# Performance work log

Measured on AMD Instinct MI355X. Metric: run time of the kernel, lower is better.

Reference implementation:

```python
import jax, jax.numpy as jnp
import numpy as np

B, T, C = 16, 2048, 384
E = 8          # num_experts
TOP_K = 2
CAP_F = 1.0
D_FF = 4 * C   # 1536


def setup_inputs() -> dict:
    key = jax.random.key(0)
    ks = jax.random.split(key, 10)
    s = 0.02
    return {
        "x": jax.random.normal(ks[0], (B, T, C), dtype=jnp.float32),
        "noise": jax.random.normal(ks[1], (B, T, E), dtype=jnp.float32),
        "w_route": jax.random.normal(ks[2], (C, E), dtype=jnp.float32) * s,
        "b_route": jnp.zeros((E,), dtype=jnp.float32),
        "w_noise": jax.random.normal(ks[3], (C, E), dtype=jnp.float32) * s,
        "b_noise": jnp.zeros((E,), dtype=jnp.float32),
        "w1": jax.random.normal(ks[4], (E, C, D_FF), dtype=jnp.float32) * s,
        "b1": jnp.zeros((E, D_FF), dtype=jnp.float32),
        "w2": jax.random.normal(ks[5], (E, D_FF, C), dtype=jnp.float32) * s,
        "b2": jnp.zeros((E, C), dtype=jnp.float32),
    }


def _moe_forward(x, noise, w_route, b_route, w_noise, b_noise, w1, b1, w2, b2):
    Bx, Tx, Cx = x.shape
    N = Bx * Tx
    cap = int(N * TOP_K / E * CAP_F)  # static expert capacity

    # --- NoisyTopkRouter ---
    logits = jnp.einsum('btc,ce->bte', x, w_route) + b_route
    noise_logits = jnp.einsum('btc,ce->bte', x, w_noise) + b_noise
    noisy = logits + noise * jax.nn.softplus(noise_logits)
    topv, topi = jax.lax.top_k(noisy, TOP_K)                    # [B,T,K]
    keep_mask = jnp.any(jax.nn.one_hot(topi, E, dtype=jnp.bool_), axis=-2)  # [B,T,E]
    sparse_logits = jnp.where(keep_mask, noisy, -jnp.inf)
    gating = jax.nn.softmax(sparse_logits, axis=-1)             # [B,T,E]

    # --- dispatch by top-1 expert with capacity drop (eval: dropout off) ---
    flat_x = x.reshape(N, Cx)
    flat_g = gating.reshape(N, E)
    top1 = jnp.argmax(flat_g, axis=-1)                          # [N]
    token_ids = jnp.arange(N, dtype=jnp.int32)
    out = jnp.zeros_like(flat_x)

    for i in range(E):
        mask = top1 == i                                        # [N]
        pos = jnp.cumsum(mask) - 1                              # rank within expert
        keep = mask & (pos < cap)
        slot = jnp.where(keep, pos, cap)                        # overflow -> dummy slot
        buf = jnp.zeros((cap + 1,), dtype=jnp.int32).at[slot].set(token_ids)
        idx = buf[:cap]                                         # token id per capacity slot
        valid = (jnp.arange(cap) < jnp.sum(keep))[:, None]      # [cap,1]
        xi = flat_x[idx]                                        # [cap,C] gather
        h = jnp.square(jax.nn.relu(xi @ w1[i] + b1[i]))         # ReLU^2
        yi = h @ w2[i] + b2[i]                                  # [cap,C]
        weighted = yi * flat_g[idx, i][:, None] * valid
        out = out.at[idx].add(weighted)                         # scatter-add

    return out.reshape(Bx, Tx, Cx)


def reference(x, noise, w_route, b_route, w_noise, b_noise, w1, b1, w2, b2):
    return _moe_forward(x, noise, w_route, b_route, w_noise, b_noise, w1, b1, w2, b2)
```

## Files before the change

kernel.cpp:

```cpp
#include <hip/hip_runtime.h>
#include <stdint.h>

#define E_NUM 8
#define CAP 8192
#define NTOK 32768
#define CDIM 384
#define DFF 1536
#define CNT_PAD 64

typedef unsigned short u16;
typedef __attribute__((ext_vector_type(8))) short short8;
typedef __attribute__((ext_vector_type(4))) float f32x4;

__device__ inline u16 f2bf(float f) {
    uint32_t u = __builtin_bit_cast(uint32_t, f);
    u += 0x7fffu + ((u >> 16) & 1u);
    return (u16)(u >> 16);
}

__device__ inline void gload_lds16(const void* g, void* l) {
    __builtin_amdgcn_global_load_lds(
        (const __attribute__((address_space(1))) void*)(uintptr_t)g,
        (__attribute__((address_space(3))) void*)(uint32_t)(uintptr_t)l,
        16, 0, 0);
}

__device__ inline void expert_span(const int* __restrict__ cnt, int e,
                                   int& base, int& n_e) {
    base = 0; n_e = 0;
#pragma unroll
    for (int i = 0; i < E_NUM; ++i) {
        int n = min(cnt[i * CNT_PAD], CAP);
        if (i < e) base += (n + 127) & ~127;
        else if (i == e) n_e = n;
    }
}

#define RT_TOK 64
#define RT_KC 64
#define RT_XS 68

__global__ __launch_bounds__(256, 4) void routing_kernel(
    const float* __restrict__ x, const float* __restrict__ noise,
    const float* __restrict__ w_route, const float* __restrict__ b_route,
    const float* __restrict__ w_noise, const float* __restrict__ b_noise,
    int* __restrict__ cnt, int* __restrict__ list, float* __restrict__ gate,
    u16* __restrict__ xbf)
{
    __shared__ float xs[RT_TOK * RT_XS];
    int tid = threadIdx.x;
    int lane = tid & 63;
    int seg = __builtin_amdgcn_readfirstlane(tid >> 6);
    int tok = tid & 63;
    int t0 = blockIdx.x * RT_TOK;

    int srow = tid >> 4;
    int scol = (tid & 15) * 4;

    float ar[E_NUM], an[E_NUM];
#pragma unroll
    for (int e = 0; e < E_NUM; ++e) { ar[e] = 0.f; an[e] = 0.f; }

    for (int c = 0; c < CDIM / RT_KC; ++c) {
        __syncthreads();
#pragma unroll
        for (int p = 0; p < 4; ++p) {
            int row = p * 16 + srow;
            float4 v = *(const float4*)(x + (size_t)(t0 + row) * CDIM + c * RT_KC + scol);
            *(float4*)&xs[row * RT_XS + scol] = v;
            uint2 b;
            b.x = (uint32_t)f2bf(v.x) | ((uint32_t)f2bf(v.y) << 16);
            b.y = (uint32_t)f2bf(v.z) | ((uint32_t)f2bf(v.w) << 16);
            *(uint2*)(xbf + (size_t)(t0 + row) * CDIM + c * RT_KC + scol) = b;
        }
        __syncthreads();
#pragma unroll
        for (int q = 0; q < 4; ++q) {
            float4 xq = *(const float4*)&xs[tok * RT_XS + seg * 16 + q * 4];
            int kb = c * RT_KC + seg * 16 + q * 4;
#pragma unroll
            for (int jj = 0; jj < 4; ++jj) {
                const float* wrk = w_route + (size_t)(kb + jj) * E_NUM;
                const float* wnk = w_noise + (size_t)(kb + jj) * E_NUM;
                float4 wa = *(const float4*)wrk, wb = *(const float4*)(wrk + 4);
                float4 na = *(const float4*)wnk, nb = *(const float4*)(wnk + 4);
                float xk = (jj == 0) ? xq.x : (jj == 1) ? xq.y : (jj == 2) ? xq.z : xq.w;
                ar[0] += xk * wa.x; ar[1] += xk * wa.y; ar[2] += xk * wa.z; ar[3] += xk * wa.w;
                ar[4] += xk * wb.x; ar[5] += xk * wb.y; ar[6] += xk * wb.z; ar[7] += xk * wb.w;
                an[0] += xk * na.x; an[1] += xk * na.y; an[2] += xk * na.z; an[3] += xk * na.w;
                an[4] += xk * nb.x; an[5] += xk * nb.y; an[6] += xk * nb.z; an[7] += xk * nb.w;
            }
        }
    }
    __syncthreads();
    float* part = xs;
    float* pp = part + (size_t)(seg * 64 + tok) * 16;
    *(f32x4*)&pp[0]  = (f32x4){ar[0], ar[1], ar[2], ar[3]};
    *(f32x4*)&pp[4]  = (f32x4){ar[4], ar[5], ar[6], ar[7]};
    *(f32x4*)&pp[8]  = (f32x4){an[0], an[1], an[2], an[3]};
    *(f32x4*)&pp[12] = (f32x4){an[4], an[5], an[6], an[7]};
    __syncthreads();
    if (seg == 0) {
        int t = t0 + lane;
        float sr[E_NUM], sn[E_NUM];
#pragma unroll
        for (int e = 0; e < E_NUM; ++e) { sr[e] = b_route[e]; sn[e] = b_noise[e]; }
#pragma unroll
        for (int s = 0; s < 4; ++s) {
            const float* q = part + (size_t)(s * 64 + lane) * 16;
#pragma unroll
            for (int e = 0; e < E_NUM; ++e) { sr[e] += q[e]; sn[e] += q[8 + e]; }
        }
        float nz[E_NUM];
        const float* np = noise + (size_t)t * E_NUM;
#pragma unroll
        for (int e = 0; e < E_NUM; ++e) {
            float s = sn[e];
            float sp = fmaxf(s, 0.f) + __logf(1.f + __expf(-fabsf(s)));
            nz[e] = sr[e] + np[e] * sp;
        }
        float v1 = -1e30f; int i1 = 0;
#pragma unroll
        for (int e = 0; e < E_NUM; ++e) if (nz[e] > v1) { v1 = nz[e]; i1 = e; }
        float v2 = -1e30f;
#pragma unroll
        for (int e = 0; e < E_NUM; ++e) if (e != i1 && nz[e] > v2) v2 = nz[e];
        gate[t] = 1.f / (1.f + __expf(v2 - v1));
#pragma unroll
        for (int e = 0; e < E_NUM; ++e) {
            unsigned long long m = __ballot(i1 == e);
            if (m == 0) continue;
            int cnum = __popcll(m);
            int leader = __ffsll((long long)m) - 1;
            int basec = 0;
            if (lane == leader) basec = atomicAdd(&cnt[e * CNT_PAD], cnum);
            basec = __shfl(basec, leader);
            if (i1 == e) {
                int pos = basec + __popcll(m & ((1ull << lane) - 1ull));
                if (pos < CAP) list[e * CAP + pos] = t;
            }
        }
    }
}

__global__ __launch_bounds__(256) void transpose_cvt_kernel(
    const float* __restrict__ w1, u16* __restrict__ W1t,
    const float* __restrict__ w2, u16* __restrict__ W2t)
{
    __shared__ float tile[32][33];
    int z = blockIdx.z;
    const float* in; u16* out; int R, S, r0, c0;
    if (z < E_NUM) {
        in = w1 + (size_t)z * CDIM * DFF;  out = W1t + (size_t)z * CDIM * DFF;
        R = CDIM; S = DFF;
        c0 = blockIdx.x * 32; r0 = blockIdx.y * 32;
    } else {
        in = w2 + (size_t)(z - E_NUM) * DFF * CDIM;
        out = W2t + (size_t)(z - E_NUM) * DFF * CDIM;
        R = DFF; S = CDIM;
        r0 = blockIdx.x * 32; c0 = blockIdx.y * 32;
    }
    int tx = threadIdx.x, ty = threadIdx.y;
#pragma unroll
    for (int i = ty; i < 32; i += 8)
        tile[i][tx] = in[(size_t)(r0 + i) * S + (c0 + tx)];
    __syncthreads();
#pragma unroll
    for (int i = ty; i < 32; i += 8)
        out[(size_t)(c0 + i) * R + (r0 + tx)] = f2bf(tile[tx][i]);
}

template <int KD, int ND, bool FFN1>
__global__ __launch_bounds__(256, 2) void gemm_kernel(
    const u16* __restrict__ A, const u16* __restrict__ Bt,
    const float* __restrict__ bias, u16* __restrict__ H, float* __restrict__ Out,
    const int* __restrict__ cnt, const int* __restrict__ list,
    const float* __restrict__ gate)
{
    constexpr int NT = ND / 128;
    int bid = blockIdx.x;
    int xcd = bid & 7, slot = bid >> 3;
    int n_idx = slot % NT;
    int mglob = xcd + 8 * (slot / NT);
    int e = mglob >> 6;
    int m0 = (mglob & 63) * 128;
    int base, n_e;
    expert_span(cnt, e, base, n_e);
    int pad_e = (n_e + 127) & ~127;
    if (m0 >= pad_e) return;
    const u16* Be = Bt + ((size_t)e * ND + (size_t)n_idx * 128) * KD;

    __shared__ __align__(16) u16 As[2][128 * 64];
    __shared__ __align__(16) u16 Bs[2][128 * 64];
    __shared__ int s_tok[128];

    int tid = threadIdx.x;
    int w = tid >> 6, lane = tid & 63;
    int quad = lane >> 4, l15 = lane & 15;
    int wr = w & 1, wc = w >> 1;

    int srow = tid >> 3;
    int gcol = ((tid & 7) ^ ((tid >> 3) & 7)) * 8;

    if (FFN1) {
        if (tid < 128) {
            int rr = m0 + tid;
            s_tok[tid] = (rr < n_e) ? list[(size_t)e * CAP + rr] : NTOK;
        }
        __syncthreads();
    }
    const u16* Arow[4];
#pragma unroll
    for (int i = 0; i < 4; ++i) {
        int row = i * 32 + srow;
        if (FFN1) Arow[i] = A + (size_t)s_tok[row] * KD;
        else      Arow[i] = A + (size_t)(base + m0 + row) * KD;
    }

    auto stage = [&](int buf, int kb) {
#pragma unroll
        for (int i = 0; i < 4; ++i) {
            gload_lds16(Arow[i] + kb * 64 + gcol, &As[buf][i * 2048 + tid * 8]);
            gload_lds16(Be + (size_t)(i * 32 + srow) * KD + kb * 64 + gcol,
                        &Bs[buf][i * 2048 + tid * 8]);
        }
    };

    f32x4 acc[4][4];
    f32x4 zero = {0.f, 0.f, 0.f, 0.f};
#pragma unroll
    for (int a = 0; a < 4; ++a)
#pragma unroll
        for (int b = 0; b < 4; ++b) acc[a][b] = zero;

    constexpr int NK = KD / 64;
    stage(0, 0);
#pragma unroll 2
    for (int kb = 0; kb < NK; ++kb) {
        const int cur = kb & 1;
        if (kb + 1 < NK) {
            stage(cur ^ 1, kb + 1);
            asm volatile("s_waitcnt vmcnt(8)" ::: "memory");
        } else {
            asm volatile("s_waitcnt vmcnt(0)" ::: "memory");
        }
        __builtin_amdgcn_s_barrier();
        __builtin_amdgcn_sched_barrier(0);
#pragma unroll
        for (int h = 0; h < 2; ++h) {
            int pga = (((h * 4 + quad) ^ (l15 & 7))) * 8;
            short8 af[4], bf[4];
#pragma unroll
            for (int t = 0; t < 4; ++t) {
                af[t] = *(const short8*)&As[cur][(wr * 64 + t * 16 + l15) * 64 + pga];
                bf[t] = *(const short8*)&Bs[cur][(wc * 64 + t * 16 + l15) * 64 + pga];
            }
#pragma unroll
            for (int mt = 0; mt < 4; ++mt)
#pragma unroll
                for (int nt = 0; nt < 4; ++nt)
                    acc[mt][nt] = __builtin_amdgcn_mfma_f32_16x16x32_bf16(
                        af[mt], bf[nt], acc[mt][nt], 0, 0, 0);
        }
        __builtin_amdgcn_sched_barrier(0);
        __builtin_amdgcn_s_barrier();
        __builtin_amdgcn_sched_barrier(0);
    }

    int n0 = n_idx * 128;
    if (FFN1) {
        u16* Hs = (u16*)&As[0][0];
#pragma unroll
        for (int mt = 0; mt < 4; ++mt) {
            int rowL = wr * 64 + mt * 16 + quad * 4;
#pragma unroll
            for (int nt = 0; nt < 4; ++nt) {
                int colL = wc * 64 + nt * 16 + l15;
                float b = bias[(size_t)e * ND + n0 + colL];
#pragma unroll
                for (int r = 0; r < 4; ++r) {
                    float v = acc[mt][nt][r] + b;
                    v = fmaxf(v, 0.f);
                    int row = rowL + r;
                    Hs[row * 128 + (colL ^ ((row & 7) << 3))] = f2bf(v * v);
                }
            }
        }
        __syncthreads();
        u16* He = H + (size_t)(base + m0) * ND + n0;
#pragma unroll
        for (int j = 0; j < 8; ++j) {
            int idx = tid + j * 256;
            int row = idx >> 4;
            int c8 = (idx & 15) * 8;
            *(f32x4*)(He + (size_t)row * ND + c8) =
                *(const f32x4*)(Hs + row * 128 + (c8 ^ ((row & 7) << 3)));
        }
    } else {
#pragma unroll
        for (int mt = 0; mt < 4; ++mt) {
            int rowL = wr * 64 + mt * 16 + quad * 4;
#pragma unroll
            for (int r = 0; r < 4; ++r) {
                int rr = m0 + rowL + r;
                if (rr < n_e) {
                    int tok = list[(size_t)e * CAP + rr];
                    float g = gate[tok];
#pragma unroll
                    for (int nt = 0; nt < 4; ++nt) {
                        int col = n0 + wc * 64 + nt * 16 + l15;
                        float v = acc[mt][nt][r] + bias[(size_t)e * ND + col];
                        Out[(size_t)tok * CDIM + col] = v * g;
                    }
                }
            }
        }
    }
}

extern "C" void kernel_launch(void* const* d_in, const int* in_sizes, int n_in,
                              void* d_out, int out_size, void* d_ws, size_t ws_size,
                              hipStream_t stream)
{
    const float* x       = (const float*)d_in[0];
    const float* noise   = (const float*)d_in[1];
    const float* w_route = (const float*)d_in[2];
    const float* b_route = (const float*)d_in[3];
    const float* w_noise = (const float*)d_in[4];
    const float* b_noise = (const float*)d_in[5];
    const float* w1      = (const float*)d_in[6];
    const float* b1      = (const float*)d_in[7];
    const float* w2      = (const float*)d_in[8];
    const float* b2      = (const float*)d_in[9];
    float* out = (float*)d_out;

    char* ws = (char*)d_ws;
    size_t off = 0;
    auto alloc = [&](size_t bytes) {
        char* p = ws + off;
        off += (bytes + 255) & ~(size_t)255;
        return p;
    };
    int*   cnt  = (int*)alloc((size_t)E_NUM * CNT_PAD * sizeof(int));
    int*   list = (int*)alloc((size_t)E_NUM * CAP * sizeof(int));
    float* gate = (float*)alloc((size_t)NTOK * sizeof(float));
    u16*   W1t  = (u16*)alloc((size_t)E_NUM * DFF * CDIM * 2);
    u16*   W2t  = (u16*)alloc((size_t)E_NUM * CDIM * DFF * 2);

    u16* Xbf = (u16*)alloc((size_t)(NTOK + 1) * CDIM * 2);
    size_t rows = NTOK + E_NUM * 128;
    u16* Hb = (u16*)alloc(rows * DFF * 2);

    hipMemsetAsync(cnt, 0, (size_t)E_NUM * CNT_PAD * sizeof(int), stream);
    hipMemsetAsync(Xbf + (size_t)NTOK * CDIM, 0, CDIM * 2, stream);

    routing_kernel<<<NTOK / RT_TOK, 256, 0, stream>>>(x, noise, w_route, b_route,
                                                      w_noise, b_noise, cnt, list, gate, Xbf);
    transpose_cvt_kernel<<<dim3(48, 12, 16), dim3(32, 8), 0, stream>>>(w1, W1t, w2, W2t);

    gemm_kernel<CDIM, DFF, true><<<dim3((DFF / 128) * 512), 256, 0, stream>>>(
        Xbf, W1t, b1, Hb, nullptr, cnt, list, nullptr);
    gemm_kernel<DFF, CDIM, false><<<dim3((CDIM / 128) * 512), 256, 0, stream>>>(
        Hb, W2t, b2, nullptr, out, cnt, list, gate);
}
```

Baseline: 305.0 us.

## Fuse both expert FFN GEMMs into one kernel keeping hidden tile in LDS

Replaces the two separate expert GEMM launches with a single fused kernel. Each 512-thread block owns a 128-token tile and loops over the hidden dimension in 128-wide chunks: it computes the ReLU^2 hidden chunk into LDS, then immediately accumulates the second projection into a full 128x384 register accumulator, loading W2 fragments directly from global memory. This removes the round trip of the large bf16 hidden buffer through HBM and one launch. In exchange the grid shrinks to at most 512 blocks with heavy register use and a serialized per-chunk schedule, so occupancy and latency hiding may suffer.

```diff
diff --git a/kernel.cpp b/kernel.cpp
--- a/kernel.cpp
+++ b/kernel.cpp
@@ -170,148 +170,181 @@
         out[(size_t)(c0 + i) * R + (r0 + tx)] = f2bf(tile[tx][i]);
 }
 
-template <int KD, int ND, bool FFN1>
-__global__ __launch_bounds__(256, 2) void gemm_kernel(
-    const u16* __restrict__ A, const u16* __restrict__ Bt,
-    const float* __restrict__ bias, u16* __restrict__ H, float* __restrict__ Out,
+__global__ __launch_bounds__(512, 2) void moe_ffn_kernel(
+    const u16* __restrict__ Xbf, const u16* __restrict__ W1t,
+    const u16* __restrict__ W2t, const float* __restrict__ b1,
+    const float* __restrict__ b2, float* __restrict__ Out,
     const int* __restrict__ cnt, const int* __restrict__ list,
     const float* __restrict__ gate)
 {
-    constexpr int NT = ND / 128;
     int bid = blockIdx.x;
     int xcd = bid & 7, slot = bid >> 3;
-    int n_idx = slot % NT;
-    int mglob = xcd + 8 * (slot / NT);
+    int mglob = xcd + 8 * slot;
     int e = mglob >> 6;
     int m0 = (mglob & 63) * 128;
     int base, n_e;
     expert_span(cnt, e, base, n_e);
+    (void)base;
     int pad_e = (n_e + 127) & ~127;
     if (m0 >= pad_e) return;
-    const u16* Be = Bt + ((size_t)e * ND + (size_t)n_idx * 128) * KD;
 
     __shared__ __align__(16) u16 As[2][128 * 64];
     __shared__ __align__(16) u16 Bs[2][128 * 64];
+    __shared__ __align__(16) u16 Hs[128 * 128];
     __shared__ int s_tok[128];
 
     int tid = threadIdx.x;
     int w = tid >> 6, lane = tid & 63;
     int quad = lane >> 4, l15 = lane & 15;
-    int wr = w & 1, wc = w >> 1;
+    int wr = w & 1;
+    int wc = w >> 1;
 
     int srow = tid >> 3;
-    int gcol = ((tid & 7) ^ ((tid >> 3) & 7)) * 8;
-
-    if (FFN1) {
-        if (tid < 128) {
-            int rr = m0 + tid;
-            s_tok[tid] = (rr < n_e) ? list[(size_t)e * CAP + rr] : NTOK;
-        }
-        __syncthreads();
-    }
-    const u16* Arow[4];
-#pragma unroll
-    for (int i = 0; i < 4; ++i) {
-        int row = i * 32 + srow;
-        if (FFN1) Arow[i] = A + (size_t)s_tok[row] * KD;
-        else      Arow[i] = A + (size_t)(base + m0 + row) * KD;
-    }
-
-    auto stage = [&](int buf, int kb) {
-#pragma unroll
-        for (int i = 0; i < 4; ++i) {
-            gload_lds16(Arow[i] + kb * 64 + gcol, &As[buf][i * 2048 + tid * 8]);
-            gload_lds16(Be + (size_t)(i * 32 + srow) * KD + kb * 64 + gcol,
-                        &Bs[buf][i * 2048 + tid * 8]);
+    int gcol = ((tid & 7) ^ (srow & 7)) * 8;
+
+    if (tid < 128) {
+        int rr = m0 + tid;
+        s_tok[tid] = (rr < n_e) ? list[(size_t)e * CAP + rr] : NTOK;
+    }
+    __syncthreads();
+
+    const u16* Arow[2];
+#pragma unroll
+    for (int i = 0; i < 2; ++i)
+        Arow[i] = Xbf + (size_t)s_tok[i * 64 + srow] * CDIM;
+    const u16* W1e = W1t + (size_t)e * DFF * CDIM;
+    const u16* W2e = W2t + (size_t)e * CDIM * DFF;
+
+    auto stage = [&](int buf, int d, int kb) {
+#pragma unroll
+        for (int i = 0; i < 2; ++i) {
+            int row = i * 64 + srow;
+            gload_lds16(Arow[i] + kb * 64 + gcol, &As[buf][i * 4096 + tid * 8]);
+            gload_lds16(W1e + (size_t)(d * 128 + row) * CDIM + kb * 64 + gcol,
+                        &Bs[buf][i * 4096 + tid * 8]);
         }
     };
 
-    f32x4 acc[4][4];
+    f32x4 accY[4][6];
     f32x4 zero = {0.f, 0.f, 0.f, 0.f};
 #pragma unroll
     for (int a = 0; a < 4; ++a)
 #pragma unroll
-        for (int b = 0; b < 4; ++b) acc[a][b] = zero;
-
-    constexpr int NK = KD / 64;
-    stage(0, 0);
-#pragma unroll 2
-    for (int kb = 0; kb < NK; ++kb) {
-        const int cur = kb & 1;
-        if (kb + 1 < NK) {
-            stage(cur ^ 1, kb + 1);
-            asm volatile("s_waitcnt vmcnt(8)" ::: "memory");
-        } else {
-            asm volatile("s_waitcnt vmcnt(0)" ::: "memory");
-        }
-        __builtin_amdgcn_s_barrier();
-        __builtin_amdgcn_sched_barrier(0);
-#pragma unroll
-        for (int h = 0; h < 2; ++h) {
-            int pga = (((h * 4 + quad) ^ (l15 & 7))) * 8;
-            short8 af[4], bf[4];
-#pragma unroll
-            for (int t = 0; t < 4; ++t) {
-                af[t] = *(const short8*)&As[cur][(wr * 64 + t * 16 + l15) * 64 + pga];
-                bf[t] = *(const short8*)&Bs[cur][(wc * 64 + t * 16 + l15) * 64 + pga];
-            }
-#pragma unroll
-            for (int mt = 0; mt < 4; ++mt)
-#pragma unroll
-                for (int nt = 0; nt < 4; ++nt)
-                    acc[mt][nt] = __builtin_amdgcn_mfma_f32_16x16x32_bf16(
-                        af[mt], bf[nt], acc[mt][nt], 0, 0, 0);
-        }
-        __builtin_amdgcn_sched_barrier(0);
-        __builtin_amdgcn_s_barrier();
-        __builtin_amdgcn_sched_barrier(0);
-    }
-
-    int n0 = n_idx * 128;
-    if (FFN1) {
-        u16* Hs = (u16*)&As[0][0];
-#pragma unroll
-        for (int mt = 0; mt < 4; ++mt) {
-            int rowL = wr * 64 + mt * 16 + quad * 4;
-#pragma unroll
-            for (int nt = 0; nt < 4; ++nt) {
-                int colL = wc * 64 + nt * 16 + l15;
-                float b = bias[(size_t)e * ND + n0 + colL];
+        for (int b = 0; b < 6; ++b) accY[a][b] = zero;
+
+    int n0Y = wc * 96;
+
+    stage(0, 0, 0);
+    int buf = 0;
+    for (int d = 0; d < DFF / 128; ++d) {
+        f32x4 acc1[4][2];
+#pragma unroll
+        for (int a = 0; a < 4; ++a)
+#pragma unroll
+            for (int b = 0; b < 2; ++b) acc1[a][b] = zero;
+
+        for (int kb = 0; kb < 6; ++kb) {
+            if (kb < 5)            stage(buf ^ 1, d, kb + 1);
+            else if (d < 11)       stage(buf ^ 1, d + 1, 0);
+            if (kb < 5 || d < 11) { asm volatile("s_waitcnt vmcnt(4)" ::: "memory"); }
+            else                  { asm volatile("s_waitcnt vmcnt(0)" ::: "memory"); }
+            __builtin_amdgcn_s_barrier();
+            __builtin_amdgcn_sched_barrier(0);
+#pragma unroll
+            for (int h = 0; h < 2; ++h) {
+                int pga = ((h * 4 + quad) ^ (l15 & 7)) * 8;
+                short8 af[4], bf[2];
+#pragma unroll
+                for (int t = 0; t < 4; ++t)
+                    af[t] = *(const short8*)&As[buf][(wr * 64 + t * 16 + l15) * 64 + pga];
+#pragma unroll
+                for (int t = 0; t < 2; ++t)
+                    bf[t] = *(const short8*)&Bs[buf][(wc * 32 + t * 16 + l15) * 64 + pga];
+#pragma unroll
+                for (int mt = 0; mt < 4; ++mt)
+#pragma unroll
+                    for (int nt = 0; nt < 2; ++nt)
+                        acc1[mt][nt] = __builtin_amdgcn_mfma_f32_16x16x32_bf16(
+                            af[mt], bf[nt], acc1[mt][nt], 0, 0, 0);
+            }
+            __builtin_amdgcn_sched_barrier(0);
+            __builtin_amdgcn_s_barrier();
+            __builtin_amdgcn_sched_barrier(0);
+            buf ^= 1;
+        }
+
+#pragma unroll
+        for (int nt = 0; nt < 2; ++nt) {
+            int colL = wc * 32 + nt * 16 + l15;
+            float bb = b1[(size_t)e * DFF + d * 128 + colL];
+#pragma unroll
+            for (int mt = 0; mt < 4; ++mt) {
+                int rowB = wr * 64 + mt * 16 + quad * 4;
 #pragma unroll
                 for (int r = 0; r < 4; ++r) {
-                    float v = acc[mt][nt][r] + b;
+                    float v = acc1[mt][nt][r] + bb;
                     v = fmaxf(v, 0.f);
-                    int row = rowL + r;
+                    int row = rowB + r;
                     Hs[row * 128 + (colL ^ ((row & 7) << 3))] = f2bf(v * v);
                 }
             }
         }
-        __syncthreads();
-        u16* He = H + (size_t)(base + m0) * ND + n0;
-#pragma unroll
-        for (int j = 0; j < 8; ++j) {
-            int idx = tid + j * 256;
-            int row = idx >> 4;
-            int c8 = (idx & 15) * 8;
-            *(f32x4*)(He + (size_t)row * ND + c8) =
-                *(const f32x4*)(Hs + row * 128 + (c8 ^ ((row & 7) << 3)));
-        }
-    } else {
-#pragma unroll
-        for (int mt = 0; mt < 4; ++mt) {
-            int rowL = wr * 64 + mt * 16 + quad * 4;
-#pragma unroll
-            for (int r = 0; r < 4; ++r) {
-                int rr = m0 + rowL + r;
-                if (rr < n_e) {
-                    int tok = list[(size_t)e * CAP + rr];
-                    float g = gate[tok];
-#pragma unroll
-                    for (int nt = 0; nt < 4; ++nt) {
-                        int col = n0 + wc * 64 + nt * 16 + l15;
-                        float v = acc[mt][nt][r] + bias[(size_t)e * ND + col];
-                        Out[(size_t)tok * CDIM + col] = v * g;
-                    }
+        __builtin_amdgcn_s_barrier();
+
+        short8 Bf0[6], Bf1[6];
+#pragma unroll
+        for (int nf = 0; nf < 6; ++nf)
+            Bf0[nf] = *(const short8*)(W2e + (size_t)(n0Y + nf * 16 + l15) * DFF
+                                       + d * 128 + 0 * 32 + quad * 8);
+#pragma unroll
+        for (int ks = 0; ks < 4; ++ks) {
+            if (ks < 3) {
+                if (ks & 1) {
+#pragma unroll
+                    for (int nf = 0; nf < 6; ++nf)
+                        Bf0[nf] = *(const short8*)(W2e + (size_t)(n0Y + nf * 16 + l15) * DFF
+                                                   + d * 128 + (ks + 1) * 32 + quad * 8);
+                } else {
+#pragma unroll
+                    for (int nf = 0; nf < 6; ++nf)
+                        Bf1[nf] = *(const short8*)(W2e + (size_t)(n0Y + nf * 16 + l15) * DFF
+                                                   + d * 128 + (ks + 1) * 32 + quad * 8);
+                }
+                asm volatile("s_waitcnt vmcnt(6)" ::: "memory");
+            } else {
+                asm volatile("s_waitcnt vmcnt(0)" ::: "memory");
+            }
+            short8 af2[4];
+#pragma unroll
+            for (int mf = 0; mf < 4; ++mf) {
+                int row = wr * 64 + mf * 16 + l15;
+                int col = (ks * 32 + quad * 8) ^ ((l15 & 7) << 3);
+                af2[mf] = *(const short8*)&Hs[row * 128 + col];
+            }
+#pragma unroll
+            for (int mf = 0; mf < 4; ++mf)
+#pragma unroll
+                for (int nf = 0; nf < 6; ++nf)
+                    accY[mf][nf] = __builtin_amdgcn_mfma_f32_16x16x32_bf16(
+                        af2[mf], (ks & 1) ? Bf1[nf] : Bf0[nf], accY[mf][nf], 0, 0, 0);
+        }
+    }
+
+#pragma unroll
+    for (int mf = 0; mf < 4; ++mf) {
+        int rowB = wr * 64 + mf * 16 + quad * 4;
+#pragma unroll
+        for (int r = 0; r < 4; ++r) {
+            int rowL = rowB + r;
+            int rr = m0 + rowL;
+            if (rr < n_e) {
+                int tok = s_tok[rowL];
+                float g = gate[tok];
+#pragma unroll
+                for (int nf = 0; nf < 6; ++nf) {
+                    int col = n0Y + nf * 16 + l15;
+                    float v = accY[mf][nf][r] + b2[(size_t)e * CDIM + col];
+                    Out[(size_t)tok * CDIM + col] = v * g;
                 }
             }
         }
@@ -346,10 +379,7 @@
     float* gate = (float*)alloc((size_t)NTOK * sizeof(float));
     u16*   W1t  = (u16*)alloc((size_t)E_NUM * DFF * CDIM * 2);
     u16*   W2t  = (u16*)alloc((size_t)E_NUM * CDIM * DFF * 2);
-
-    u16* Xbf = (u16*)alloc((size_t)(NTOK + 1) * CDIM * 2);
-    size_t rows = NTOK + E_NUM * 128;
-    u16* Hb = (u16*)alloc(rows * DFF * 2);
+    u16*   Xbf  = (u16*)alloc((size_t)(NTOK + 1) * CDIM * 2);
 
     hipMemsetAsync(cnt, 0, (size_t)E_NUM * CNT_PAD * sizeof(int), stream);
     hipMemsetAsync(Xbf + (size_t)NTOK * CDIM, 0, CDIM * 2, stream);
@@ -358,8 +388,6 @@
                                                       w_noise, b_noise, cnt, list, gate, Xbf);
     transpose_cvt_kernel<<<dim3(48, 12, 16), dim3(32, 8), 0, stream>>>(w1, W1t, w2, W2t);
 
-    gemm_kernel<CDIM, DFF, true><<<dim3((DFF / 128) * 512), 256, 0, stream>>>(
-        Xbf, W1t, b1, Hb, nullptr, cnt, list, nullptr);
-    gemm_kernel<DFF, CDIM, false><<<dim3((CDIM / 128) * 512), 256, 0, stream>>>(
-        Hb, W2t, b2, nullptr, out, cnt, list, gate);
-}
+    moe_ffn_kernel<<<512, 512, 0, stream>>>(Xbf, W1t, W2t, b1, b2, out,
+                                            cnt, list, gate);
+}
```

New measurement: 415.4 us. 36.2% more time.
